# Performance work log

Hardware: AMD Instinct MI355X
Metric: run time of the kernel (lower is better)

Reference implementation:

```python
import jax, jax.numpy as jnp
import numpy as np

H = 1024
B = 8192

def setup_inputs() -> dict:
    key = jax.random.key(0)
    ks = jax.random.split(key, 8)
    s = 1.0 / np.sqrt(H)
    return {
        "x": jax.random.normal(ks[0], (B, H), jnp.float32),
        "h": jax.random.normal(ks[1], (B, H), jnp.float32),
        "W_ih_w": jax.random.normal(ks[2], (3 * H, H), jnp.float32) * s,
        "W_ih_b": jax.random.normal(ks[3], (3 * H,), jnp.float32) * s,
        "U_r_w": jax.random.normal(ks[4], (H, H), jnp.float32) * s,
        "U_z_w": jax.random.normal(ks[5], (H, H), jnp.float32) * s,
        "U_n_w": jax.random.normal(ks[6], (H, H), jnp.float32) * s,
        "U_n_b": jax.random.normal(ks[7], (H,), jnp.float32) * s,
    }

def reference(x, h, W_ih_w, W_ih_b, U_r_w, U_z_w, U_n_w, U_n_b):
    # fused input projection: (B, 3H)
    x_proj = x @ W_ih_w.T + W_ih_b
    r_x, z_x, n_x = jnp.split(x_proj, 3, axis=-1)
    # per-gate hidden matmuls (transpose_U=False path)
    r_h = h @ U_r_w.T
    z_h = h @ U_z_w.T
    n_h = h @ U_n_w.T + U_n_b
    r = jax.nn.sigmoid(r_x + r_h)
    z = jax.nn.sigmoid(z_x + z_h)
    n = jnp.tanh(n_x + r * n_h)
    return (1.0 - z) * n + z * h
```

## Files before the change

kernel.cpp:

```cpp
#include <hip/hip_runtime.h>
#include <hip/hip_bf16.h>
#include <cstdint>

#define HDIM 1024
#define BM 256
#define BN 64
#define BKK 32
#define NT (HDIM / BKK)

typedef __attribute__((ext_vector_type(8))) __bf16 bf16x8;
typedef __attribute__((ext_vector_type(8))) unsigned short u16x8;
typedef __attribute__((ext_vector_type(4))) float f32x4;

static __device__ __forceinline__ unsigned short f2b(float f) {
    __hip_bfloat16 h = __float2bfloat16(f);
    return __builtin_bit_cast(unsigned short, h);
}

static __device__ __forceinline__ void barrier_fence() {
    asm volatile("" ::: "memory");
    __builtin_amdgcn_s_barrier();
    asm volatile("" ::: "memory");
}

__global__ void __launch_bounds__(256) cvt_all(
    const float* __restrict__ x, const float* __restrict__ h,
    const float* __restrict__ wih, const float* __restrict__ ur,
    const float* __restrict__ uz, const float* __restrict__ un,
    unsigned short* __restrict__ wb, unsigned short* __restrict__ urb,
    unsigned short* __restrict__ uzb, unsigned short* __restrict__ unb,
    unsigned short* __restrict__ xb, unsigned short* __restrict__ hb) {
    int b = blockIdx.x;
    const float* src; unsigned short* dst; int idx;
    if (b < 3072)       { src = wih; dst = wb;  idx = b; }
    else if (b < 4096)  { src = ur;  dst = urb; idx = b - 3072; }
    else if (b < 5120)  { src = uz;  dst = uzb; idx = b - 4096; }
    else if (b < 6144)  { src = un;  dst = unb; idx = b - 5120; }
    else if (b < 14336) { src = x;   dst = xb;  idx = b - 6144; }
    else                { src = h;   dst = hb;  idx = b - 14336; }
    int i = idx * 256 + threadIdx.x;
    float4 v = ((const float4*)src)[i];
    ushort4 o;
    o.x = f2b(v.x); o.y = f2b(v.y); o.z = f2b(v.z); o.w = f2b(v.w);
    ((ushort4*)dst)[i] = o;
}

template<int MH, int NF>
__device__ __forceinline__ void mm_cluster(f32x4 (&acc)[4][4][2],
        const bf16x8 (&ax)[4], const bf16x8 (&ah)[4], const bf16x8 (&bq)[6]) {
#pragma unroll
    for (int mi = 0; mi < 6; ++mi) {
        const int g = (mi == 0 || mi == 3) ? 0 : (mi == 1 || mi == 4) ? 1 : (mi == 2) ? 2 : 3;
#pragma unroll
        for (int m2 = 0; m2 < 2; ++m2) {
            const int mf = MH * 2 + m2;
            acc[g][mf][NF] = __builtin_amdgcn_mfma_f32_16x16x32_bf16(
                (mi < 3) ? ax[mf] : ah[mf], bq[mi], acc[g][mf][NF], 0, 0, 0);
        }
    }
}

__global__ void __launch_bounds__(512, 2)
gru_fused8(const float* __restrict__ hg,
           const unsigned short* __restrict__ xb, const unsigned short* __restrict__ hb,
           const unsigned short* __restrict__ wih,
           const unsigned short* __restrict__ ur,
           const unsigned short* __restrict__ uz,
           const unsigned short* __restrict__ un,
           const float* __restrict__ bih, const float* __restrict__ bun,
           float* __restrict__ out) {
    __shared__ __align__(16) unsigned short smem[2][28672];

    const int tid  = threadIdx.x;
    const int lane = tid & 63;
    const int wv   = tid >> 6;
    const int wm   = wv >> 1;
    const int wn   = wv & 1;
    const int lr   = lane & 15;
    const int ls   = lane >> 4;
    const int sel  = (lr >> 1) & 3;
    const int fo   = (ls ^ sel) << 3;

    const int bid = blockIdx.x;
    const int swz = (bid & 7) * 64 + (bid >> 3);
    const int m0  = (swz & 31) * BM;
    const int n0  = (swz >> 5) * BN;

    const unsigned short* wb6[6] = {
        wih + (size_t)n0 * HDIM,
        wih + (size_t)(HDIM + n0) * HDIM,
        wih + (size_t)(2 * HDIM + n0) * HDIM,
        ur  + (size_t)n0 * HDIM,
        uz  + (size_t)n0 * HDIM,
        un  + (size_t)n0 * HDIM
    };

    f32x4 acc[4][4][2];
#pragma unroll
    for (int g = 0; g < 4; ++g)
#pragma unroll
        for (int mf = 0; mf < 4; ++mf)
#pragma unroll
            for (int nf = 0; nf < 2; ++nf)
                acc[g][mf][nf] = f32x4{0.f, 0.f, 0.f, 0.f};

    auto STAGE_W = [&](unsigned short* nb, int kt) {
        const int k0 = kt * BKK;
#pragma unroll
        for (int l = 0; l < 3; ++l) {
            const int id = l * 512 + tid;
            const int mi = id >> 8;
            const int c  = id & 255;
            const int r  = c >> 2;
            const int sl = (c & 3) ^ ((c >> 3) & 3);
            const unsigned short* g = wb6[mi] + (size_t)r * HDIM + k0 + sl * 8;
            __builtin_amdgcn_global_load_lds(
                (const __attribute__((address_space(1))) void*)g,
                (__attribute__((address_space(3))) void*)(nb + 16384 + l * 4096 + wv * 512),
                16, 0, 0);
        }
    };
    auto STAGE_X = [&](unsigned short* nb, int kt) {
        const int k0 = kt * BKK;
#pragma unroll
        for (int half = 0; half < 2; ++half) {
            const int c  = half * 512 + tid;
            const int r  = c >> 2;
            const int sl = (c & 3) ^ ((c >> 3) & 3);
            const unsigned short* g = xb + (size_t)(m0 + r) * HDIM + k0 + sl * 8;
            __builtin_amdgcn_global_load_lds(
                (const __attribute__((address_space(1))) void*)g,
                (__attribute__((address_space(3))) void*)(nb + half * 4096 + wv * 512),
                16, 0, 0);
        }
    };
    auto STAGE_H = [&](unsigned short* nb, int kt) {
        const int k0 = kt * BKK;
#pragma unroll
        for (int half = 0; half < 2; ++half) {
            const int c  = half * 512 + tid;
            const int r  = c >> 2;
            const int sl = (c & 3) ^ ((c >> 3) & 3);
            const unsigned short* g = hb + (size_t)(m0 + r) * HDIM + k0 + sl * 8;
            __builtin_amdgcn_global_load_lds(
                (const __attribute__((address_space(1))) void*)g,
                (__attribute__((address_space(3))) void*)(nb + 8192 + half * 4096 + wv * 512),
                16, 0, 0);
        }
    };

    auto TILE = [&](int cur, int ktn, bool stage) {
        const unsigned short* sb = &smem[cur][0];
        unsigned short* nb = &smem[cur ^ 1][0];
        bf16x8 ax[4], ah[4], bq[6];

        {
            const int ra0 = (wm * 64 + 0 * 16 + lr) * 32 + fo;
            const int ra1 = (wm * 64 + 1 * 16 + lr) * 32 + fo;
            ax[0] = *(const bf16x8*)(sb + ra0);
            ah[0] = *(const bf16x8*)(sb + 8192 + ra0);
            ax[1] = *(const bf16x8*)(sb + ra1);
            ah[1] = *(const bf16x8*)(sb + 8192 + ra1);
            const int rb = (wn * 32 + 0 * 16 + lr) * 32 + fo;
#pragma unroll
            for (int mi = 0; mi < 6; ++mi)
                bq[mi] = *(const bf16x8*)(sb + 16384 + mi * 2048 + rb);
        }
        if (stage) STAGE_W(nb, ktn);
        barrier_fence();
        asm volatile("s_waitcnt lgkmcnt(0)" ::: "memory");
        __builtin_amdgcn_sched_barrier(0);
        __builtin_amdgcn_s_setprio(1);
        mm_cluster<0, 0>(acc, ax, ah, bq);
        __builtin_amdgcn_s_setprio(0);
        barrier_fence();

        {
            const int ra2 = (wm * 64 + 2 * 16 + lr) * 32 + fo;
            const int ra3 = (wm * 64 + 3 * 16 + lr) * 32 + fo;
            ax[2] = *(const bf16x8*)(sb + ra2);
            ah[2] = *(const bf16x8*)(sb + 8192 + ra2);
            ax[3] = *(const bf16x8*)(sb + ra3);
            ah[3] = *(const bf16x8*)(sb + 8192 + ra3);
        }
        if (stage) STAGE_X(nb, ktn);
        barrier_fence();
        asm volatile("s_waitcnt lgkmcnt(0)" ::: "memory");
        __builtin_amdgcn_sched_barrier(0);
        __builtin_amdgcn_s_setprio(1);
        mm_cluster<1, 0>(acc, ax, ah, bq);
        __builtin_amdgcn_s_setprio(0);
        barrier_fence();

        {
            const int rb = (wn * 32 + 1 * 16 + lr) * 32 + fo;
#pragma unroll
            for (int mi = 0; mi < 6; ++mi)
                bq[mi] = *(const bf16x8*)(sb + 16384 + mi * 2048 + rb);
        }
        if (stage) STAGE_H(nb, ktn);
        barrier_fence();
        asm volatile("s_waitcnt lgkmcnt(0)" ::: "memory");
        __builtin_amdgcn_sched_barrier(0);
        __builtin_amdgcn_s_setprio(1);
        mm_cluster<0, 1>(acc, ax, ah, bq);
        __builtin_amdgcn_s_setprio(0);
        barrier_fence();

        __builtin_amdgcn_s_setprio(1);
        mm_cluster<1, 1>(acc, ax, ah, bq);
        __builtin_amdgcn_s_setprio(0);
        asm volatile("s_waitcnt vmcnt(0)" ::: "memory");
        barrier_fence();
    };

    STAGE_W(&smem[0][0], 0);
    STAGE_X(&smem[0][0], 0);
    STAGE_H(&smem[0][0], 0);
    asm volatile("s_waitcnt vmcnt(0)" ::: "memory");
    barrier_fence();

#pragma unroll 1
    for (int t = 0; t < NT - 1; ++t)
        TILE(t & 1, t + 1, true);
    TILE((NT - 1) & 1, 0, false);

#pragma unroll
    for (int nf = 0; nf < 2; ++nf) {
        const int gc = n0 + wn * 32 + nf * 16 + lr;
        const float br  = bih[gc];
        const float bz  = bih[HDIM + gc];
        const float bnx = bih[2 * HDIM + gc];
        const float bn2 = bun[gc];
#pragma unroll
        for (int mf = 0; mf < 4; ++mf) {
#pragma unroll
            for (int rr = 0; rr < 4; ++rr) {
                const int gr = m0 + wm * 64 + mf * 16 + ls * 4 + rr;
                const float rv = 1.f / (1.f + __expf(-(acc[0][mf][nf][rr] + br)));
                const float zv = 1.f / (1.f + __expf(-(acc[1][mf][nf][rr] + bz)));
                const float nv = tanhf(acc[2][mf][nf][rr] + bnx + rv * (acc[3][mf][nf][rr] + bn2));
                const float hv = hg[(size_t)gr * HDIM + gc];
                out[(size_t)gr * HDIM + gc] = (1.f - zv) * nv + zv * hv;
            }
        }
    }
}

__global__ void __launch_bounds__(256, 2)
gru_fused_fb(const float* __restrict__ hg,
             const float* __restrict__ xg32, const float* __restrict__ hg32,
             const unsigned short* __restrict__ wih,
             const unsigned short* __restrict__ ur,
             const unsigned short* __restrict__ uz,
             const unsigned short* __restrict__ un,
             const float* __restrict__ bih, const float* __restrict__ bun,
             float* __restrict__ out) {
    __shared__ __align__(16) unsigned short smem[2][20480];
    const int tid  = threadIdx.x;
    const int lane = tid & 63;
    const int wv   = tid >> 6;
    const int wm   = wv >> 1;
    const int wn   = wv & 1;
    const int lr   = lane & 15;
    const int ls   = lane >> 4;
    const int m0   = blockIdx.y * 128;
    const int n0   = blockIdx.x * BN;

    const unsigned short* wb6[6] = {
        wih + (size_t)n0 * HDIM, wih + (size_t)(HDIM + n0) * HDIM,
        wih + (size_t)(2 * HDIM + n0) * HDIM, ur + (size_t)n0 * HDIM,
        uz + (size_t)n0 * HDIM, un + (size_t)n0 * HDIM
    };
    const int wr  = tid >> 2;
    const int wsl = (tid & 3) ^ ((tid >> 3) & 3);

    f32x4 acc[4][4][2];
#pragma unroll
    for (int g = 0; g < 4; ++g)
#pragma unroll
        for (int mf = 0; mf < 4; ++mf)
#pragma unroll
            for (int nf = 0; nf < 2; ++nf)
                acc[g][mf][nf] = f32x4{0.f, 0.f, 0.f, 0.f};

    auto STAGE = [&](int bufi, int kt) {
        const int k0 = kt * BKK;
        unsigned short* sb = &smem[bufi][0];
        float4 fx[2][2], fh[2][2];
#pragma unroll
        for (int half = 0; half < 2; ++half) {
            const int c2 = half * 256 + tid;
            const int r2 = c2 >> 2;
            const int sl = c2 & 3;
            const float* gx = xg32 + (size_t)(m0 + r2) * HDIM + k0 + sl * 8;
            const float* gh = hg32 + (size_t)(m0 + r2) * HDIM + k0 + sl * 8;
            fx[half][0] = ((const float4*)gx)[0];
            fx[half][1] = ((const float4*)gx)[1];
            fh[half][0] = ((const float4*)gh)[0];
            fh[half][1] = ((const float4*)gh)[1];
        }
#pragma unroll
        for (int mi = 0; mi < 6; ++mi) {
            const unsigned short* g = wb6[mi] + (size_t)wr * HDIM + k0 + wsl * 8;
            __builtin_amdgcn_global_load_lds(
                (const __attribute__((address_space(1))) void*)g,
                (__attribute__((address_space(3))) void*)(sb + 8192 + mi * 2048 + wv * 512),
                16, 0, 0);
        }
#pragma unroll
        for (int half = 0; half < 2; ++half) {
            const int c2 = half * 256 + tid;
            const int r2 = c2 >> 2;
            const int sp = (c2 & 3) ^ ((c2 >> 3) & 3);
            u16x8 px, ph;
#pragma unroll
            for (int q = 0; q < 4; ++q) {
                px[q]     = f2b(fx[half][0][q]);
                px[q + 4] = f2b(fx[half][1][q]);
                ph[q]     = f2b(fh[half][0][q]);
                ph[q + 4] = f2b(fh[half][1][q]);
            }
            *(u16x8*)(sb + r2 * 32 + sp * 8)        = px;
            *(u16x8*)(sb + 4096 + r2 * 32 + sp * 8) = ph;
        }
    };
    auto COMPUTE = [&](int bufi) {
        const unsigned short* sb = &smem[bufi][0];
        const int sel = (lr >> 1) & 3;
        const int fo  = (ls ^ sel) << 3;
        bf16x8 ax[4], ah[4];
#pragma unroll
        for (int mf = 0; mf < 4; ++mf) {
            const int row = wm * 64 + mf * 16 + lr;
            ax[mf] = *(const bf16x8*)(sb + row * 32 + fo);
            ah[mf] = *(const bf16x8*)(sb + 4096 + row * 32 + fo);
        }
#pragma unroll
        for (int mi = 0; mi < 6; ++mi) {
            const unsigned short* wt = sb + 8192 + mi * 2048;
            bf16x8 b0 = *(const bf16x8*)(wt + (wn * 32 + lr) * 32 + fo);
            bf16x8 b1 = *(const bf16x8*)(wt + (wn * 32 + 16 + lr) * 32 + fo);
            const int g = (mi == 0 || mi == 3) ? 0 : (mi == 1 || mi == 4) ? 1 : (mi == 2) ? 2 : 3;
            const bf16x8* a = (mi < 3) ? ax : ah;
#pragma unroll
            for (int mf = 0; mf < 4; ++mf) {
                acc[g][mf][0] = __builtin_amdgcn_mfma_f32_16x16x32_bf16(a[mf], b0, acc[g][mf][0], 0, 0, 0);
                acc[g][mf][1] = __builtin_amdgcn_mfma_f32_16x16x32_bf16(a[mf], b1, acc[g][mf][1], 0, 0, 0);
            }
        }
    };
    auto WAITN = [&]() { asm volatile("s_waitcnt vmcnt(6) lgkmcnt(0)" ::: "memory"); };

    STAGE(0, 0);
#pragma unroll 1
    for (int kt = 0; kt < NT - 2; kt += 2) {
        STAGE(1, kt + 1); WAITN(); barrier_fence();
        COMPUTE(0);       barrier_fence();
        STAGE(0, kt + 2); WAITN(); barrier_fence();
        COMPUTE(1);       barrier_fence();
    }
    STAGE(1, NT - 1); WAITN(); barrier_fence();
    COMPUTE(0);       barrier_fence();
    asm volatile("s_waitcnt vmcnt(0) lgkmcnt(0)" ::: "memory");
    __builtin_amdgcn_s_barrier();
    asm volatile("" ::: "memory");
    COMPUTE(1);

#pragma unroll
    for (int nf = 0; nf < 2; ++nf) {
        const int gc = n0 + wn * 32 + nf * 16 + lr;
        const float br  = bih[gc];
        const float bz  = bih[HDIM + gc];
        const float bnx = bih[2 * HDIM + gc];
        const float bn2 = bun[gc];
#pragma unroll
        for (int mf = 0; mf < 4; ++mf) {
#pragma unroll
            for (int rr = 0; rr < 4; ++rr) {
                const int gr = m0 + wm * 64 + mf * 16 + ls * 4 + rr;
                const float rv = 1.f / (1.f + __expf(-(acc[0][mf][nf][rr] + br)));
                const float zv = 1.f / (1.f + __expf(-(acc[1][mf][nf][rr] + bz)));
                const float nv = tanhf(acc[2][mf][nf][rr] + bnx + rv * (acc[3][mf][nf][rr] + bn2));
                const float hv = hg[(size_t)gr * HDIM + gc];
                out[(size_t)gr * HDIM + gc] = (1.f - zv) * nv + zv * hv;
            }
        }
    }
}

extern "C" void kernel_launch(void* const* d_in, const int* in_sizes, int n_in,
                              void* d_out, int out_size, void* d_ws, size_t ws_size,
                              hipStream_t stream) {
    const float* x   = (const float*)d_in[0];
    const float* h   = (const float*)d_in[1];
    const float* Wih = (const float*)d_in[2];
    const float* bih = (const float*)d_in[3];
    const float* Ur  = (const float*)d_in[4];
    const float* Uz  = (const float*)d_in[5];
    const float* Un  = (const float*)d_in[6];
    const float* bun = (const float*)d_in[7];
    float* out = (float*)d_out;

    unsigned short* wsp  = (unsigned short*)d_ws;
    unsigned short* wihb = wsp;
    unsigned short* urb  = wihb + 3 * 1024 * 1024;
    unsigned short* uzb  = urb + 1024 * 1024;
    unsigned short* unb  = uzb + 1024 * 1024;
    unsigned short* xb   = unb + 1024 * 1024;
    unsigned short* hb   = xb + 8 * 1024 * 1024;

    const bool xhb = ws_size >= 46137344ull;

    cvt_all<<<xhb ? 22528 : 6144, 256, 0, stream>>>(
        x, h, Wih, Ur, Uz, Un, wihb, urb, uzb, unb, xb, hb);

    if (xhb) {
        gru_fused8<<<512, 512, 0, stream>>>(
            h, xb, hb, wihb, urb, uzb, unb, bih, bun, out);
    } else {
        dim3 grid(HDIM / BN, 8192 / 128);
        gru_fused_fb<<<grid, 256, 0, stream>>>(
            h, x, h, wihb, urb, uzb, unb, bih, bun, out);
    }
}
```

Before: 157.8 us.

## Triple-buffer X/H tiles with prefetch distance two and partial vmcnt waits

Splits shared memory into a double-buffered weight area and a triple-buffered X/H activation area. X/H tiles are now prefetched two K-steps ahead, and the end-of-iteration wait drops from vmcnt(0) to vmcnt(4), so one activation stage stays in flight across the barrier instead of draining all global loads every tile. Global source pointers and LDS fragment offsets are computed once and advanced incrementally instead of being recomputed each stage. The cost is more LDS per block (about 144 KB) and a more fragile wait-count scheme that depends on the exact load ordering.

```diff
diff --git a/kernel.cpp b/kernel.cpp
--- a/kernel.cpp
+++ b/kernel.cpp
@@ -3,10 +3,7 @@
 #include <cstdint>
 
 #define HDIM 1024
-#define BM 256
-#define BN 64
-#define BKK 32
-#define NT (HDIM / BKK)
+#define NT 32
 
 typedef __attribute__((ext_vector_type(8))) __bf16 bf16x8;
 typedef __attribute__((ext_vector_type(8))) unsigned short u16x8;
@@ -61,15 +58,16 @@
 }
 
 __global__ void __launch_bounds__(512, 2)
-gru_fused8(const float* __restrict__ hg,
-           const unsigned short* __restrict__ xb, const unsigned short* __restrict__ hb,
-           const unsigned short* __restrict__ wih,
-           const unsigned short* __restrict__ ur,
-           const unsigned short* __restrict__ uz,
-           const unsigned short* __restrict__ un,
-           const float* __restrict__ bih, const float* __restrict__ bun,
-           float* __restrict__ out) {
-    __shared__ __align__(16) unsigned short smem[2][28672];
+gru4p(const float* __restrict__ hg,
+      const unsigned short* __restrict__ xb, const unsigned short* __restrict__ hb,
+      const unsigned short* __restrict__ wih,
+      const unsigned short* __restrict__ ur,
+      const unsigned short* __restrict__ uz,
+      const unsigned short* __restrict__ un,
+      const float* __restrict__ bih, const float* __restrict__ bun,
+      float* __restrict__ out) {
+    __shared__ __align__(16) unsigned short wlds[2][12288];
+    __shared__ __align__(16) unsigned short xhlds[3][16384];
 
     const int tid  = threadIdx.x;
     const int lane = tid & 63;
@@ -78,13 +76,11 @@
     const int wn   = wv & 1;
     const int lr   = lane & 15;
     const int ls   = lane >> 4;
-    const int sel  = (lr >> 1) & 3;
-    const int fo   = (ls ^ sel) << 3;
 
     const int bid = blockIdx.x;
     const int swz = (bid & 7) * 64 + (bid >> 3);
-    const int m0  = (swz & 31) * BM;
-    const int n0  = (swz >> 5) * BN;
+    const int m0  = (swz & 31) * 256;
+    const int n0  = (swz >> 5) * 64;
 
     const unsigned short* wb6[6] = {
         wih + (size_t)n0 * HDIM,
@@ -94,6 +90,38 @@
         uz  + (size_t)n0 * HDIM,
         un  + (size_t)n0 * HDIM
     };
+    const unsigned short* pwp[3];
+    int wdst[3];
+#pragma unroll
+    for (int l = 0; l < 3; ++l) {
+        const int id = l * 512 + tid;
+        const int mi = id >> 8;
+        const int c  = id & 255;
+        const int r  = c >> 2;
+        const int sl = (c & 3) ^ ((c >> 3) & 3);
+        pwp[l]  = wb6[mi] + (size_t)r * HDIM + sl * 8;
+        wdst[l] = mi * 2048 + (wv & 3) * 512;
+    }
+    const unsigned short* pxh[4];
+#pragma unroll
+    for (int half = 0; half < 2; ++half) {
+        const int c  = half * 512 + tid;
+        const int r  = c >> 2;
+        const int sl = (c & 3) ^ ((c >> 3) & 3);
+        pxh[half]     = xb + (size_t)(m0 + r) * HDIM + sl * 8;
+        pxh[2 + half] = hb + (size_t)(m0 + r) * HDIM + sl * 8;
+    }
+
+    int aoff[4];
+#pragma unroll
+    for (int mf = 0; mf < 4; ++mf) {
+        const int row = wm * 64 + mf * 16 + lr;
+        aoff[mf] = row * 32 + ((ls ^ ((row >> 1) & 3)) << 3);
+    }
+    const int brow0 = wn * 32 + lr;
+    const int brow1 = brow0 + 16;
+    const int boff0 = brow0 * 32 + ((ls ^ ((brow0 >> 1) & 3)) << 3);
+    const int boff1 = brow1 * 32 + ((ls ^ ((brow1 >> 1) & 3)) << 3);
 
     f32x4 acc[4][4][2];
 #pragma unroll
@@ -104,126 +132,96 @@
             for (int nf = 0; nf < 2; ++nf)
                 acc[g][mf][nf] = f32x4{0.f, 0.f, 0.f, 0.f};
 
-    auto STAGE_W = [&](unsigned short* nb, int kt) {
-        const int k0 = kt * BKK;
+    auto STAGE_W = [&](unsigned short* nb) {
 #pragma unroll
         for (int l = 0; l < 3; ++l) {
-            const int id = l * 512 + tid;
-            const int mi = id >> 8;
-            const int c  = id & 255;
-            const int r  = c >> 2;
-            const int sl = (c & 3) ^ ((c >> 3) & 3);
-            const unsigned short* g = wb6[mi] + (size_t)r * HDIM + k0 + sl * 8;
             __builtin_amdgcn_global_load_lds(
-                (const __attribute__((address_space(1))) void*)g,
-                (__attribute__((address_space(3))) void*)(nb + 16384 + l * 4096 + wv * 512),
-                16, 0, 0);
-        }
-    };
-    auto STAGE_X = [&](unsigned short* nb, int kt) {
-        const int k0 = kt * BKK;
+                (const __attribute__((address_space(1))) void*)pwp[l],
+                (__attribute__((address_space(3))) void*)(nb + wdst[l]), 16, 0, 0);
+            pwp[l] += 32;
+        }
+    };
+    auto STAGE_XH = [&](unsigned short* nb) {
 #pragma unroll
         for (int half = 0; half < 2; ++half) {
-            const int c  = half * 512 + tid;
-            const int r  = c >> 2;
-            const int sl = (c & 3) ^ ((c >> 3) & 3);
-            const unsigned short* g = xb + (size_t)(m0 + r) * HDIM + k0 + sl * 8;
             __builtin_amdgcn_global_load_lds(
-                (const __attribute__((address_space(1))) void*)g,
+                (const __attribute__((address_space(1))) void*)pxh[half],
                 (__attribute__((address_space(3))) void*)(nb + half * 4096 + wv * 512),
                 16, 0, 0);
-        }
-    };
-    auto STAGE_H = [&](unsigned short* nb, int kt) {
-        const int k0 = kt * BKK;
-#pragma unroll
-        for (int half = 0; half < 2; ++half) {
-            const int c  = half * 512 + tid;
-            const int r  = c >> 2;
-            const int sl = (c & 3) ^ ((c >> 3) & 3);
-            const unsigned short* g = hb + (size_t)(m0 + r) * HDIM + k0 + sl * 8;
+            pxh[half] += 32;
             __builtin_amdgcn_global_load_lds(
-                (const __attribute__((address_space(1))) void*)g,
+                (const __attribute__((address_space(1))) void*)pxh[2 + half],
                 (__attribute__((address_space(3))) void*)(nb + 8192 + half * 4096 + wv * 512),
                 16, 0, 0);
-        }
-    };
-
-    auto TILE = [&](int cur, int ktn, bool stage) {
-        const unsigned short* sb = &smem[cur][0];
-        unsigned short* nb = &smem[cur ^ 1][0];
-        bf16x8 ax[4], ah[4], bq[6];
-
-        {
-            const int ra0 = (wm * 64 + 0 * 16 + lr) * 32 + fo;
-            const int ra1 = (wm * 64 + 1 * 16 + lr) * 32 + fo;
-            ax[0] = *(const bf16x8*)(sb + ra0);
-            ah[0] = *(const bf16x8*)(sb + 8192 + ra0);
-            ax[1] = *(const bf16x8*)(sb + ra1);
-            ah[1] = *(const bf16x8*)(sb + 8192 + ra1);
-            const int rb = (wn * 32 + 0 * 16 + lr) * 32 + fo;
-#pragma unroll
-            for (int mi = 0; mi < 6; ++mi)
-                bq[mi] = *(const bf16x8*)(sb + 16384 + mi * 2048 + rb);
-        }
-        if (stage) STAGE_W(nb, ktn);
+            pxh[2 + half] += 32;
+        }
+    };
+
+    STAGE_XH(&xhlds[0][0]);
+    STAGE_XH(&xhlds[1][0]);
+    STAGE_W(&wlds[0][0]);
+    asm volatile("s_waitcnt vmcnt(0)" ::: "memory");
+    barrier_fence();
+
+    int xi = 0;
+#pragma unroll 1
+    for (int t = 0; t < NT; ++t) {
+        const unsigned short* xc = &xhlds[xi][0];
+        const unsigned short* wc = &wlds[t & 1][0];
+        bf16x8 ax[4], ah[4], b0[6], b1[6];
+
+        ax[0] = *(const bf16x8*)(xc + aoff[0]);
+        ax[1] = *(const bf16x8*)(xc + aoff[1]);
+        ah[0] = *(const bf16x8*)(xc + 8192 + aoff[0]);
+        ah[1] = *(const bf16x8*)(xc + 8192 + aoff[1]);
+#pragma unroll
+        for (int mi = 0; mi < 6; ++mi)
+            b0[mi] = *(const bf16x8*)(wc + mi * 2048 + boff0);
+        if (t + 1 < NT) STAGE_W(&wlds[(t + 1) & 1][0]);
         barrier_fence();
         asm volatile("s_waitcnt lgkmcnt(0)" ::: "memory");
         __builtin_amdgcn_sched_barrier(0);
         __builtin_amdgcn_s_setprio(1);
-        mm_cluster<0, 0>(acc, ax, ah, bq);
+        mm_cluster<0, 0>(acc, ax, ah, b0);
         __builtin_amdgcn_s_setprio(0);
         barrier_fence();
 
-        {
-            const int ra2 = (wm * 64 + 2 * 16 + lr) * 32 + fo;
-            const int ra3 = (wm * 64 + 3 * 16 + lr) * 32 + fo;
-            ax[2] = *(const bf16x8*)(sb + ra2);
-            ah[2] = *(const bf16x8*)(sb + 8192 + ra2);
-            ax[3] = *(const bf16x8*)(sb + ra3);
-            ah[3] = *(const bf16x8*)(sb + 8192 + ra3);
-        }
-        if (stage) STAGE_X(nb, ktn);
+        ax[2] = *(const bf16x8*)(xc + aoff[2]);
+        ax[3] = *(const bf16x8*)(xc + aoff[3]);
+        ah[2] = *(const bf16x8*)(xc + 8192 + aoff[2]);
+        ah[3] = *(const bf16x8*)(xc + 8192 + aoff[3]);
         barrier_fence();
         asm volatile("s_waitcnt lgkmcnt(0)" ::: "memory");
         __builtin_amdgcn_sched_barrier(0);
         __builtin_amdgcn_s_setprio(1);
-        mm_cluster<1, 0>(acc, ax, ah, bq);
+        mm_cluster<1, 0>(acc, ax, ah, b0);
         __builtin_amdgcn_s_setprio(0);
         barrier_fence();
 
-        {
-            const int rb = (wn * 32 + 1 * 16 + lr) * 32 + fo;
-#pragma unroll
-            for (int mi = 0; mi < 6; ++mi)
-                bq[mi] = *(const bf16x8*)(sb + 16384 + mi * 2048 + rb);
-        }
-        if (stage) STAGE_H(nb, ktn);
+#pragma unroll
+        for (int mi = 0; mi < 6; ++mi)
+            b1[mi] = *(const bf16x8*)(wc + mi * 2048 + boff1);
+        if (t + 2 < NT) {
+            int ni = xi + 2; if (ni >= 3) ni -= 3;
+            STAGE_XH(&xhlds[ni][0]);
+        }
         barrier_fence();
         asm volatile("s_waitcnt lgkmcnt(0)" ::: "memory");
         __builtin_amdgcn_sched_barrier(0);
         __builtin_amdgcn_s_setprio(1);
-        mm_cluster<0, 1>(acc, ax, ah, bq);
+        mm_cluster<0, 1>(acc, ax, ah, b1);
         __builtin_amdgcn_s_setprio(0);
         barrier_fence();
 
         __builtin_amdgcn_s_setprio(1);
-        mm_cluster<1, 1>(acc, ax, ah, bq);
+        mm_cluster<1, 1>(acc, ax, ah, b1);
         __builtin_amdgcn_s_setprio(0);
-        asm volatile("s_waitcnt vmcnt(0)" ::: "memory");
-        barrier_fence();
-    };
-
-    STAGE_W(&smem[0][0], 0);
-    STAGE_X(&smem[0][0], 0);
-    STAGE_H(&smem[0][0], 0);
-    asm volatile("s_waitcnt vmcnt(0)" ::: "memory");
-    barrier_fence();
-
-#pragma unroll 1
-    for (int t = 0; t < NT - 1; ++t)
-        TILE(t & 1, t + 1, true);
-    TILE((NT - 1) & 1, 0, false);
+        if (t + 2 < NT) { asm volatile("s_waitcnt vmcnt(4)" ::: "memory"); }
+        else            { asm volatile("s_waitcnt vmcnt(0)" ::: "memory"); }
+        barrier_fence();
+
+        if (++xi == 3) xi = 0;
+    }
 
 #pragma unroll
     for (int nf = 0; nf < 2; ++nf) {
@@ -265,7 +263,7 @@
     const int lr   = lane & 15;
     const int ls   = lane >> 4;
     const int m0   = blockIdx.y * 128;
-    const int n0   = blockIdx.x * BN;
+    const int n0   = blockIdx.x * 64;
 
     const unsigned short* wb6[6] = {
         wih + (size_t)n0 * HDIM, wih + (size_t)(HDIM + n0) * HDIM,
@@ -285,7 +283,7 @@
                 acc[g][mf][nf] = f32x4{0.f, 0.f, 0.f, 0.f};
 
     auto STAGE = [&](int bufi, int kt) {
-        const int k0 = kt * BKK;
+        const int k0 = kt * 32;
         unsigned short* sb = &smem[bufi][0];
         float4 fx[2][2], fh[2][2];
 #pragma unroll
@@ -407,19 +405,19 @@
     unsigned short* urb  = wihb + 3 * 1024 * 1024;
     unsigned short* uzb  = urb + 1024 * 1024;
     unsigned short* unb  = uzb + 1024 * 1024;
-    unsigned short* xb   = unb + 1024 * 1024;
-    unsigned short* hb   = xb + 8 * 1024 * 1024;
-
-    const bool xhb = ws_size >= 46137344ull;
-
-    cvt_all<<<xhb ? 22528 : 6144, 256, 0, stream>>>(
-        x, h, Wih, Ur, Uz, Un, wihb, urb, uzb, unb, xb, hb);
-
-    if (xhb) {
-        gru_fused8<<<512, 512, 0, stream>>>(
-            h, xb, hb, wihb, urb, uzb, unb, bih, bun, out);
+    unsigned short* xbb  = unb + 1024 * 1024;
+    unsigned short* hbb  = xbb + 8 * 1024 * 1024;
+
+    const bool big = ws_size >= 46137344ull;
+
+    cvt_all<<<big ? 22528 : 6144, 256, 0, stream>>>(
+        x, h, Wih, Ur, Uz, Un, wihb, urb, uzb, unb, xbb, hbb);
+
+    if (big) {
+        gru4p<<<512, 512, 0, stream>>>(
+            h, xbb, hbb, wihb, urb, uzb, unb, bih, bun, out);
     } else {
-        dim3 grid(HDIM / BN, 8192 / 128);
+        dim3 grid(HDIM / 64, 8192 / 128);
         gru_fused_fb<<<grid, 256, 0, stream>>>(
             h, x, h, wihb, urb, uzb, unb, bih, bun, out);
     }
```

After: 151.5 us. -4.0%, faster.
